# Kernel tuning notes

Hardware: AMD Instinct MI355X
Metric: run time of the kernel (lower is better)

The kernel has to match this reference:

```python
import jax, jax.numpy as jnp
import numpy as np

D_MODEL = 256
D_STATE = 64
NGROUPS = 2
EXPAND = 4
HEADDIM = 128
D_CONV = 4
D_INNER = EXPAND * D_MODEL              # 1024
NHEADS = D_INNER // HEADDIM             # 8
GN = NGROUPS * D_STATE                  # 128
D_IN_PROJ = 2 * D_INNER + 2 * GN + NHEADS  # 2312
EPS = 1e-5


def setup_inputs() -> dict:
    key = jax.random.key(0)
    ks = jax.random.split(key, 12)
    B, L = 2, 4096
    u = jax.random.normal(ks[0], (B, L, D_MODEL), dtype=jnp.float32)
    ln_gamma = jnp.ones((D_MODEL,), jnp.float32)
    ln_beta = jnp.zeros((D_MODEL,), jnp.float32)
    W_in = jax.random.normal(ks[1], (D_MODEL, D_IN_PROJ), jnp.float32) / np.sqrt(D_MODEL)
    conv_w = jax.random.normal(ks[2], (D_INNER + 2 * GN, D_CONV), jnp.float32) * 0.2
    conv_b = jax.random.normal(ks[3], (D_INNER + 2 * GN,), jnp.float32) * 0.02
    dt_bias = jnp.log(jnp.expm1(jax.random.uniform(ks[4], (NHEADS,), jnp.float32, 0.001, 0.1)))
    A_log = jnp.log(jax.random.uniform(ks[5], (NHEADS,), jnp.float32, 1.0, 16.0))
    D_param = jnp.ones((NHEADS,), jnp.float32)
    B_head_scale = jnp.ones((NHEADS, GN), jnp.float32) + 0.02 * jax.random.normal(ks[6], (NHEADS, GN), jnp.float32)
    rms_weight = jnp.ones((D_INNER,), jnp.float32)
    W_out = jax.random.normal(ks[7], (D_INNER, D_MODEL), jnp.float32) / np.sqrt(D_INNER)
    return dict(u=u, ln_gamma=ln_gamma, ln_beta=ln_beta, W_in=W_in, conv_w=conv_w,
                conv_b=conv_b, dt_bias=dt_bias, A_log=A_log, D_param=D_param,
                B_head_scale=B_head_scale, rms_weight=rms_weight, W_out=W_out)


def _mamba_mes(xn, W_in, conv_w, conv_b, dt_bias, A_log, D_param, B_head_scale, rms_weight, W_out):
    B, L, _ = xn.shape
    H, P, K = NHEADS, HEADDIM, D_CONV
    zxbcdt = xn @ W_in                                   # (B,L,2312)
    z = zxbcdt[..., :D_INNER]
    xBC = zxbcdt[..., D_INNER:D_INNER + D_INNER + 2 * GN]
    dt = zxbcdt[..., -H:]
    dt_pos = jax.nn.softplus(dt + dt_bias)               # (B,L,H)
    # causal depthwise conv1d + silu
    xp = jnp.pad(xBC, ((0, 0), (K - 1, 0), (0, 0)))
    conv = sum(xp[:, k:k + L, :] * conv_w[:, k] for k in range(K)) + conv_b
    xBC = jax.nn.silu(conv)
    x = xBC[..., :D_INNER]
    B_shared = xBC[..., D_INNER:D_INNER + GN]            # (B,L,GN)
    C_shared = xBC[..., D_INNER + GN:]                   # (B,L,GN)
    # MES: per-head B via diagonal scale, shared x (mean over heads) and shared C
    B_h = B_shared[:, :, None, :] * B_head_scale[None, None]          # (B,L,H,GN)
    x_shared = x.reshape(B, L, H, P).mean(axis=2)                     # (B,L,P)
    A = -jnp.exp(A_log)                                               # (H,)
    dA = jnp.exp(dt_pos * A)                                          # (B,L,H)
    # selective scan; per-head state (GN, P)
    def step(state, inp):
        dA_t, dt_t, B_t, C_t, x_t = inp   # (B,H),(B,H),(B,H,GN),(B,GN),(B,P)
        state = dA_t[:, :, None, None] * state + jnp.einsum('bh,bhn,bp->bhnp', dt_t, B_t, x_t)
        y_t = jnp.einsum('bn,bhnp->bhp', C_t, state)
        return state, y_t
    init = jnp.zeros((B, H, GN, P), xn.dtype)
    xs = (jnp.moveaxis(dA, 1, 0), jnp.moveaxis(dt_pos, 1, 0), jnp.moveaxis(B_h, 1, 0),
          jnp.moveaxis(C_shared, 1, 0), jnp.moveaxis(x_shared, 1, 0))
    _, ys = jax.lax.scan(step, init, xs)
    y = jnp.moveaxis(ys, 0, 1)                                        # (B,L,H,P)
    y = y + D_param[None, None, :, None] * x_shared[:, :, None, :]    # skip term D*x
    y = y.reshape(B, L, D_INNER)
    # gated RMSNorm: y * silu(z), then rmsnorm
    yg = y * jax.nn.silu(z)
    y = yg * jax.lax.rsqrt(jnp.mean(yg * yg, axis=-1, keepdims=True) + EPS) * rms_weight
    return y @ W_out


def reference(u, ln_gamma, ln_beta, W_in, conv_w, conv_b, dt_bias, A_log,
              D_param, B_head_scale, rms_weight, W_out):
    # pre-LayerNorm
    mu = jnp.mean(u, axis=-1, keepdims=True)
    var = jnp.mean((u - mu) ** 2, axis=-1, keepdims=True)
    xn = (u - mu) * jax.lax.rsqrt(var + EPS) * ln_gamma + ln_beta
    out = _mamba_mes(xn, W_in, conv_w, conv_b, dt_bias, A_log, D_param,
                     B_head_scale, rms_weight, W_out)
    return u + out  # dropout is identity in eval
```

## Files before the change

kernel.cpp:

```cpp
#include <hip/hip_runtime.h>
#include <math.h>

#define LN_TOK 4096
#define NB 2
#define NROWS (NB * LN_TOK)
#define DMODEL 256
#define DINNER 1024
#define NHEADS 8
#define GNN 128
#define DPROJ 2312
#define ZSTRIDE 2432
#define EPSF 1e-5f
#define NCHUNK 32
#define CHUNK 128
#define APAD 72
#define BPAD 64
#define MPAD 136
#define TT 16

typedef unsigned short u16;
typedef unsigned int u32;
typedef __attribute__((ext_vector_type(8))) short shortx8;
typedef __attribute__((ext_vector_type(4))) float floatx4;

__device__ __forceinline__ float sigmoidf_(float v) { return 1.f / (1.f + __expf(-v)); }
__device__ __forceinline__ float siluf_(float v)    { return v / (1.f + __expf(-v)); }
__device__ __forceinline__ float softplusf_(float v){ return v > 20.f ? v : log1pf(__expf(v)); }
__device__ __forceinline__ float b2f(u16 h) { return __uint_as_float(((u32)h) << 16); }
__device__ __forceinline__ u16 f2b(float f) {
    u32 u = __float_as_uint(f);
    u32 r = (u + 0x7fffu + ((u >> 16) & 1u)) >> 16;
    return (u16)r;
}
__device__ __forceinline__ void gld16(const void* g, void* l) {
    __builtin_amdgcn_global_load_lds((const __attribute__((address_space(1))) unsigned int*)g,
                                     (__attribute__((address_space(3))) unsigned int*)l, 16, 0, 0);
}

__global__ void k_ln(const float* __restrict__ u, const float* __restrict__ gam,
                     const float* __restrict__ bet, u16* __restrict__ xn) {
    int row = blockIdx.x;
    int tid = threadIdx.x;
    float v = u[(size_t)row * DMODEL + tid];
    __shared__ float s1[256], s2[256];
    s1[tid] = v; s2[tid] = v * v;
    __syncthreads();
    for (int off = 128; off > 0; off >>= 1) {
        if (tid < off) { s1[tid] += s1[tid + off]; s2[tid] += s2[tid + off]; }
        __syncthreads();
    }
    float mean = s1[0] * (1.f / DMODEL);
    float var  = s2[0] * (1.f / DMODEL) - mean * mean;
    float r = rsqrtf(var + EPSF);
    xn[(size_t)row * DMODEL + tid] = f2b((v - mean) * r * gam[tid] + bet[tid]);
}

__global__ void k_tcast(const float* __restrict__ in, u16* __restrict__ out,
                        int R, int C, int Cp) {
    __shared__ float tile[64][65];
    int c0 = blockIdx.x * 64, r0 = blockIdx.y * 64;
    int tx = threadIdx.x & 63, ty = threadIdx.x >> 6;
    for (int rr = ty; rr < 64; rr += 4) {
        int r = r0 + rr, c = c0 + tx;
        tile[rr][tx] = (r < R && c < C) ? in[(size_t)r * C + c] : 0.f;
    }
    __syncthreads();
    for (int cc = ty; cc < 64; cc += 4) {
        int c = c0 + cc, r = r0 + tx;
        if (c < Cp && r < R) out[(size_t)c * R + r] = f2b(tile[tx][cc]);
    }
}

__global__ __launch_bounds__(256) void k_gemm_bf(const u16* __restrict__ A,
                                                 const u16* __restrict__ Bt,
                                                 u16* __restrict__ C,
                                                 int K, int ldc) {
    __shared__ u16 As[128 * BPAD];
    __shared__ u16 Bs[128 * BPAD];
    int tid = threadIdx.x;
    int wave = tid >> 6, lane = tid & 63;
    int wm = wave >> 1, wn = wave & 1;
    int quad = lane >> 4, l16 = lane & 15;
    int m0 = blockIdx.y * 128, n0 = blockIdx.x * 128;
    floatx4 acc[4][4] = {};
    for (int k0 = 0; k0 < K; k0 += 64) {
#pragma unroll
        for (int p = 0; p < 4; p++) {
            int i = p * 256 + tid;
            int row = i >> 3, kk = (i & 7) << 3;
            gld16(&A[(size_t)(m0 + row) * K + k0 + kk], &As[i * 8]);
            gld16(&Bt[(size_t)(n0 + row) * K + k0 + kk], &Bs[i * 8]);
        }
        __syncthreads();
#pragma unroll
        for (int ks = 0; ks < 64; ks += 32) {
            shortx8 af[4], bfr[4];
#pragma unroll
            for (int i = 0; i < 4; i++)
                af[i] = *(shortx8*)&As[(wm * 64 + i * 16 + l16) * BPAD + ks + (quad << 3)];
#pragma unroll
            for (int j = 0; j < 4; j++)
                bfr[j] = *(shortx8*)&Bs[(wn * 64 + j * 16 + l16) * BPAD + ks + (quad << 3)];
#pragma unroll
            for (int i = 0; i < 4; i++)
#pragma unroll
                for (int j = 0; j < 4; j++)
                    acc[i][j] = __builtin_amdgcn_mfma_f32_16x16x32_bf16(af[i], bfr[j], acc[i][j], 0, 0, 0);
        }
        __syncthreads();
    }
#pragma unroll
    for (int i = 0; i < 4; i++) {
        int row = m0 + wm * 64 + i * 16 + quad * 4;
#pragma unroll
        for (int j = 0; j < 4; j++) {
            int col = n0 + wn * 64 + j * 16 + l16;
#pragma unroll
            for (int r = 0; r < 4; r++)
                C[(size_t)(row + r) * ldc + col] = f2b(acc[i][j][r]);
        }
    }
}

__global__ __launch_bounds__(256) void k_gemm2(const u16* __restrict__ A,
                                               const u16* __restrict__ Bt,
                                               float* __restrict__ C,
                                               int K, int ldc,
                                               const float* __restrict__ addC) {
    __shared__ u16 As[128 * BPAD];
    __shared__ u16 Bs[64 * BPAD];
    int tid = threadIdx.x;
    int wave = tid >> 6, lane = tid & 63;
    int wm = wave >> 1, wn = wave & 1;
    int quad = lane >> 4, l16 = lane & 15;
    int m0 = blockIdx.y * 128, n0 = blockIdx.x * 64;
    floatx4 acc[4][2] = {};
    for (int k0 = 0; k0 < K; k0 += 64) {
#pragma unroll
        for (int p = 0; p < 4; p++) {
            int i = p * 256 + tid;
            int row = i >> 3, kk = (i & 7) << 3;
            gld16(&A[(size_t)(m0 + row) * K + k0 + kk], &As[i * 8]);
        }
#pragma unroll
        for (int p = 0; p < 2; p++) {
            int i = p * 256 + tid;
            int row = i >> 3, kk = (i & 7) << 3;
            gld16(&Bt[(size_t)(n0 + row) * K + k0 + kk], &Bs[i * 8]);
        }
        __syncthreads();
#pragma unroll
        for (int ks = 0; ks < 64; ks += 32) {
            shortx8 af[4], bfr[2];
#pragma unroll
            for (int i = 0; i < 4; i++)
                af[i] = *(shortx8*)&As[(wm * 64 + i * 16 + l16) * BPAD + ks + (quad << 3)];
#pragma unroll
            for (int j = 0; j < 2; j++)
                bfr[j] = *(shortx8*)&Bs[(wn * 32 + j * 16 + l16) * BPAD + ks + (quad << 3)];
#pragma unroll
            for (int i = 0; i < 4; i++)
#pragma unroll
                for (int j = 0; j < 2; j++)
                    acc[i][j] = __builtin_amdgcn_mfma_f32_16x16x32_bf16(af[i], bfr[j], acc[i][j], 0, 0, 0);
        }
        __syncthreads();
    }
#pragma unroll
    for (int i = 0; i < 4; i++) {
        int row = m0 + wm * 64 + i * 16 + quad * 4;
#pragma unroll
        for (int j = 0; j < 2; j++) {
            int col = n0 + wn * 32 + j * 16 + l16;
#pragma unroll
            for (int r = 0; r < 4; r++) {
                size_t idx = (size_t)(row + r) * ldc + col;
                float v = acc[i][j][r];
                if (addC) v += addC[idx];
                C[idx] = v;
            }
        }
    }
}

#define LDW 1296
__global__ __launch_bounds__(256) void k_conv(const u16* __restrict__ zxb,
                                              const float* __restrict__ cw,
                                              const float* __restrict__ cb,
                                              const float* __restrict__ dt_bias,
                                              const float* __restrict__ A_log,
                                              u16* __restrict__ xsh, u16* __restrict__ Bsh,
                                              u16* __restrict__ Csh, u16* __restrict__ XT,
                                              u16* __restrict__ BT,
                                              float* __restrict__ dtp, float* __restrict__ laa) {
    int blk = blockIdx.x;
    int b = blk / (LN_TOK / TT), tile = blk % (LN_TOK / TT);
    int t0 = tile * TT;
    int tid = threadIdx.x;
    __shared__ u16 ld[(TT + 3) * LDW];
    __shared__ float sv[TT][260];
    __shared__ u16 bcv[TT][132];

    for (int i = tid; i < (TT + 3) * 161; i += 256) {
        int r = i / 161, ch = (i % 161) * 8;
        int t = t0 - 3 + r;
        int4 v = make_int4(0, 0, 0, 0);
        if (t >= 0)
            v = *(const int4*)&zxb[((size_t)(b * LN_TOK + t)) * ZSTRIDE + DINNER + ch];
        *(int4*)&ld[r * LDW + ch] = v;
    }

    int cmap[5];
#pragma unroll
    for (int k = 0; k < 4; k++) cmap[k] = (tid >> 7) * 512 + (tid & 127) + 128 * k;
    cmap[4] = 1024 + tid;
    float w0[5], w1[5], w2[5], w3[5], bias[5];
#pragma unroll
    for (int k = 0; k < 5; k++) {
        int c = cmap[k];
        w0[k] = cw[c * 4 + 0]; w1[k] = cw[c * 4 + 1];
        w2[k] = cw[c * 4 + 2]; w3[k] = cw[c * 4 + 3];
        bias[k] = cb[c];
    }
    float dtb = 0.f, negA = 0.f;
    if (tid < NHEADS) { dtb = dt_bias[tid]; negA = -__expf(A_log[tid]); }

    __syncthreads();

    float h1[5], h2[5], h3[5];
#pragma unroll
    for (int k = 0; k < 5; k++) {
        h3[k] = b2f(ld[0 * LDW + cmap[k]]);
        h2[k] = b2f(ld[1 * LDW + cmap[k]]);
        h1[k] = b2f(ld[2 * LDW + cmap[k]]);
    }

    for (int m = 0; m < TT; m++) {
        int t = t0 + m;
        size_t rowp = (size_t)(b * LN_TOK + t) * GNN;
        float xpart = 0.f;
#pragma unroll
        for (int k = 0; k < 5; k++) {
            float cur = b2f(ld[(m + 3) * LDW + cmap[k]]);
            float conv = bias[k] + w3[k] * cur + w2[k] * h1[k] + w1[k] * h2[k] + w0[k] * h3[k];
            h3[k] = h2[k]; h2[k] = h1[k]; h1[k] = cur;
            float s = siluf_(conv);
            if (k < 4) xpart += s;
            else {
                u16 sb = f2b(s);
                if (tid < 128) { Bsh[rowp + tid] = sb; bcv[m][tid] = sb; }
                else           Csh[rowp + tid - 128] = sb;
            }
        }
        sv[m][tid] = xpart;
        if (tid < NHEADS) {
            float dtv = b2f(ld[(m + 3) * LDW + 1280 + tid]) + dtb;
            float dp = softplusf_(dtv);
            size_t idx = ((size_t)(b * NHEADS + tid)) * LN_TOK + t;
            dtp[idx] = dp;
            laa[idx] = negA * dp;
        }
    }
    __syncthreads();

    for (int idx = tid; idx < TT * 128; idx += 256) {
        int m = idx >> 7, p = idx & 127;
        xsh[(size_t)(b * LN_TOK + t0 + m) * GNN + p] =
            f2b((sv[m][p] + sv[m][p + 128]) * 0.125f);
    }
    {
        int p = tid & 127, tg = tid >> 7;
        u16 ox[8], ob[8];
#pragma unroll
        for (int j = 0; j < 8; j++) {
            int m = tg * 8 + j;
            ox[j] = f2b((sv[m][p] + sv[m][p + 128]) * 0.125f);
            ob[j] = bcv[m][p];
        }
        size_t base = ((size_t)(b * GNN + p)) * LN_TOK + t0 + tg * 8;
        int4 vx = make_int4((u32)ox[0] | ((u32)ox[1] << 16), (u32)ox[2] | ((u32)ox[3] << 16),
                            (u32)ox[4] | ((u32)ox[5] << 16), (u32)ox[6] | ((u32)ox[7] << 16));
        int4 vb = make_int4((u32)ob[0] | ((u32)ob[1] << 16), (u32)ob[2] | ((u32)ob[3] << 16),
                            (u32)ob[4] | ((u32)ob[5] << 16), (u32)ob[6] | ((u32)ob[7] << 16));
        *(int4*)&XT[base] = vx;
        *(int4*)&BT[base] = vb;
    }
}

__global__ void k_prefix(const float* __restrict__ laa, float* __restrict__ gcum) {
    int blk = blockIdx.x;
    int bh = blk / NCHUNK, c = blk % NCHUNK;
    int tid = threadIdx.x;
    __shared__ float s[128];
    size_t base = (size_t)bh * LN_TOK + c * CHUNK;
    s[tid] = laa[base + tid];
    __syncthreads();
    for (int off = 1; off < 128; off <<= 1) {
        float v = (tid >= off) ? s[tid - off] : 0.f;
        __syncthreads();
        s[tid] += v;
        __syncthreads();
    }
    gcum[base + tid] = s[tid];
}

__global__ __launch_bounds__(256) void k_chunkS(const u16* __restrict__ BT,
                                                const u16* __restrict__ XT,
                                                const float* __restrict__ scale,
                                                const float* __restrict__ gcum,
                                                const float* __restrict__ dtp,
                                                u16* __restrict__ states) {
    int blk = blockIdx.x;
    int c = blk & 31, h = (blk >> 5) & 7, b = blk >> 8;
    int t0 = c * CHUNK;
    __shared__ u16 As[128 * APAD];
    __shared__ u16 Bs[128 * APAD];
    __shared__ float esc[128], scl[128];
    int tid = threadIdx.x;
    int wave = tid >> 6, lane = tid & 63;
    int wm = wave >> 1, wn = wave & 1;
    int quad = lane >> 4, l16 = lane & 15;
    size_t bhbase = (size_t)(b * NHEADS + h) * LN_TOK + t0;
    if (tid < 128) {
        float gl = gcum[bhbase + 127];
        esc[tid] = __expf(gl - gcum[bhbase + tid]) * dtp[bhbase + tid];
        scl[tid] = scale[h * GNN + tid];
    }
    __syncthreads();
    floatx4 acc[4][4] = {};
    size_t tbase = (size_t)(b * GNN) * LN_TOK + t0;
    for (int k0 = 0; k0 < 128; k0 += 64) {
#pragma unroll
        for (int p = 0; p < 4; p++) {
            int i = p * 256 + tid;
            int row = i >> 3, kk = (i & 7) << 3;
            int4 raw = *(const int4*)&BT[tbase + (size_t)row * LN_TOK + k0 + kk];
            u16* rp = (u16*)&raw;
            float sr = scl[row];
            u32 w[4];
#pragma unroll
            for (int q = 0; q < 4; q++) {
                u16 a  = f2b(b2f(rp[2 * q])     * sr * esc[k0 + kk + 2 * q]);
                u16 bb = f2b(b2f(rp[2 * q + 1]) * sr * esc[k0 + kk + 2 * q + 1]);
                w[q] = (u32)a | ((u32)bb << 16);
            }
            *(int4*)&As[row * APAD + kk] = make_int4(w[0], w[1], w[2], w[3]);
            *(int4*)&Bs[row * APAD + kk] = *(const int4*)&XT[tbase + (size_t)row * LN_TOK + k0 + kk];
        }
        __syncthreads();
#pragma unroll
        for (int ks = 0; ks < 64; ks += 32) {
            shortx8 af[4], bfr[4];
#pragma unroll
            for (int i = 0; i < 4; i++)
                af[i] = *(shortx8*)&As[(wm * 64 + i * 16 + l16) * APAD + ks + (quad << 3)];
#pragma unroll
            for (int j = 0; j < 4; j++)
                bfr[j] = *(shortx8*)&Bs[(wn * 64 + j * 16 + l16) * APAD + ks + (quad << 3)];
#pragma unroll
            for (int i = 0; i < 4; i++)
#pragma unroll
                for (int j = 0; j < 4; j++)
                    acc[i][j] = __builtin_amdgcn_mfma_f32_16x16x32_bf16(af[i], bfr[j], acc[i][j], 0, 0, 0);
        }
        __syncthreads();
    }
    size_t sbase = (size_t)blk * 16384;
#pragma unroll
    for (int i = 0; i < 4; i++) {
        int n0 = wm * 64 + i * 16 + quad * 4;
#pragma unroll
        for (int j = 0; j < 4; j++) {
            int p = wn * 64 + j * 16 + l16;
            u16 o[4];
#pragma unroll
            for (int r = 0; r < 4; r++) o[r] = f2b(acc[i][j][r]);
            u32 lo = (u32)o[0] | ((u32)o[1] << 16);
            u32 hi = (u32)o[2] | ((u32)o[3] << 16);
            *(uint2*)&states[sbase + (size_t)p * CHUNK + n0] = make_uint2(lo, hi);
        }
    }
}

__global__ void k_scan(u16* __restrict__ states, const float* __restrict__ gcum) {
    int idx = blockIdx.x * 256 + threadIdx.x;
    int bh = idx >> 12;
    int np = (idx & 4095) * 4;
    float r0 = 0.f, r1 = 0.f, r2 = 0.f, r3 = 0.f;
    size_t base = (size_t)bh * NCHUNK * 16384 + np;
    size_t gb = (size_t)bh * LN_TOK;
    for (int c = 0; c < NCHUNK; c++) {
        float G = __expf(gcum[gb + c * CHUNK + 127]);
        uint2 v = *(uint2*)&states[base + (size_t)c * 16384];
        float l0 = b2f((u16)(v.x & 0xffff)), l1 = b2f((u16)(v.x >> 16));
        float l2 = b2f((u16)(v.y & 0xffff)), l3 = b2f((u16)(v.y >> 16));
        uint2 o;
        o.x = (u32)f2b(r0) | ((u32)f2b(r1) << 16);
        o.y = (u32)f2b(r2) | ((u32)f2b(r3) << 16);
        *(uint2*)&states[base + (size_t)c * 16384] = o;
        r0 = G * r0 + l0; r1 = G * r1 + l1; r2 = G * r2 + l2; r3 = G * r3 + l3;
    }
}

__global__ __launch_bounds__(256) void k_chunkMY(const u16* __restrict__ Bsh,
                                                 const u16* __restrict__ Csh,
                                                 const float* __restrict__ scale,
                                                 const u16* __restrict__ states,
                                                 const u16* __restrict__ XT,
                                                 const float* __restrict__ gcum,
                                                 const float* __restrict__ dtp,
                                                 u16* __restrict__ y) {
    int blk = blockIdx.x;
    int c = blk & 31, h = (blk >> 5) & 7, b = blk >> 8;
    int t0 = c * CHUNK;
    __shared__ u16 As[128 * APAD];
    __shared__ u16 Bs[128 * APAD];
    __shared__ u16 Mt[128 * MPAD];
    __shared__ float g[128], dts[128], sc[128], eg[128];
    int tid = threadIdx.x;
    int wave = tid >> 6, lane = tid & 63;
    int wm = wave >> 1, wn = wave & 1;
    int quad = lane >> 4, l16 = lane & 15;
    size_t bhbase = (size_t)(b * NHEADS + h) * LN_TOK + t0;
    if (tid < 128) {
        float gv = gcum[bhbase + tid];
        g[tid] = gv;
        eg[tid] = __expf(gv);
        dts[tid] = dtp[bhbase + tid];
        sc[tid] = scale[h * GNN + tid];
    }
    __syncthreads();
    floatx4 acc[4][4] = {};
    size_t rbase = (size_t)(b * LN_TOK + t0) * GNN;
    for (int k0 = 0; k0 < 128; k0 += 64) {
#pragma unroll
        for (int p = 0; p < 4; p++) {
            int i = p * 256 + tid;
            int row = i >> 3, kk = (i & 7) << 3;
            int4 raw = *(const int4*)&Bsh[rbase + (size_t)row * GNN + k0 + kk];
            u16* rp = (u16*)&raw;
            u32 w[4];
#pragma unroll
            for (int q = 0; q < 4; q++) {
                u16 a  = f2b(b2f(rp[2 * q])     * sc[k0 + kk + 2 * q]);
                u16 bb = f2b(b2f(rp[2 * q + 1]) * sc[k0 + kk + 2 * q + 1]);
                w[q] = (u32)a | ((u32)bb << 16);
            }
            *(int4*)&As[row * APAD + kk] = make_int4(w[0], w[1], w[2], w[3]);
            *(int4*)&Bs[row * APAD + kk] = *(const int4*)&Csh[rbase + (size_t)row * GNN + k0 + kk];
        }
        __syncthreads();
#pragma unroll
        for (int ks = 0; ks < 64; ks += 32) {
            shortx8 af[4], bfr[4];
#pragma unroll
            for (int i = 0; i < 4; i++)
                af[i] = *(shortx8*)&As[(wm * 64 + i * 16 + l16) * APAD + ks + (quad << 3)];
#pragma unroll
            for (int j = 0; j < 4; j++)
                bfr[j] = *(shortx8*)&Bs[(wn * 64 + j * 16 + l16) * APAD + ks + (quad << 3)];
#pragma unroll
            for (int i = 0; i < 4; i++)
#pragma unroll
                for (int j = 0; j < 4; j++)
                    acc[i][j] = __builtin_amdgcn_mfma_f32_16x16x32_bf16(af[i], bfr[j], acc[i][j], 0, 0, 0);
        }
        __syncthreads();
    }
#pragma unroll
    for (int i = 0; i < 4; i++) {
        int s0 = wm * 64 + i * 16 + quad * 4;
#pragma unroll
        for (int j = 0; j < 4; j++) {
            int t = wn * 64 + j * 16 + l16;
            u16 o[4];
#pragma unroll
            for (int r = 0; r < 4; r++) {
                int s = s0 + r;
                float v = (s <= t) ? acc[i][j][r] * __expf(g[t] - g[s]) * dts[s] : 0.f;
                o[r] = f2b(v);
            }
            u32 lo = (u32)o[0] | ((u32)o[1] << 16);
            u32 hi = (u32)o[2] | ((u32)o[3] << 16);
            *(uint2*)&Mt[t * MPAD + s0] = make_uint2(lo, hi);
            acc[i][j] = (floatx4){0.f, 0.f, 0.f, 0.f};
        }
    }
    __syncthreads();
    size_t sbase = (size_t)blk * 16384;
    for (int k0 = 0; k0 < 128; k0 += 64) {
#pragma unroll
        for (int p = 0; p < 4; p++) {
            int i = p * 256 + tid;
            int row = i >> 3, kk = (i & 7) << 3;
            int4 raw = *(const int4*)&Csh[rbase + (size_t)row * GNN + k0 + kk];
            float e = eg[row];
            u16* rp = (u16*)&raw;
            u32 w[4];
#pragma unroll
            for (int q = 0; q < 4; q++) {
                u16 a  = f2b(b2f(rp[2 * q]) * e);
                u16 bb = f2b(b2f(rp[2 * q + 1]) * e);
                w[q] = (u32)a | ((u32)bb << 16);
            }
            *(int4*)&As[row * APAD + kk] = make_int4(w[0], w[1], w[2], w[3]);
            *(int4*)&Bs[row * APAD + kk] = *(const int4*)&states[sbase + (size_t)row * CHUNK + k0 + kk];
        }
        __syncthreads();
#pragma unroll
        for (int ks = 0; ks < 64; ks += 32) {
            shortx8 af[4], bfr[4];
#pragma unroll
            for (int i = 0; i < 4; i++)
                af[i] = *(shortx8*)&As[(wm * 64 + i * 16 + l16) * APAD + ks + (quad << 3)];
#pragma unroll
            for (int j = 0; j < 4; j++)
                bfr[j] = *(shortx8*)&Bs[(wn * 64 + j * 16 + l16) * APAD + ks + (quad << 3)];
#pragma unroll
            for (int i = 0; i < 4; i++)
#pragma unroll
                for (int j = 0; j < 4; j++)
                    acc[i][j] = __builtin_amdgcn_mfma_f32_16x16x32_bf16(af[i], bfr[j], acc[i][j], 0, 0, 0);
        }
        __syncthreads();
    }
    size_t xtb = (size_t)(b * GNN) * LN_TOK + t0;
    for (int k0 = 0; k0 < 128; k0 += 64) {
#pragma unroll
        for (int p = 0; p < 4; p++) {
            int i = p * 256 + tid;
            int row = i >> 3, kk = (i & 7) << 3;
            *(int4*)&Bs[row * APAD + kk] = *(const int4*)&XT[xtb + (size_t)row * LN_TOK + k0 + kk];
        }
        __syncthreads();
#pragma unroll
        for (int ks = 0; ks < 64; ks += 32) {
            shortx8 af[4], bfr[4];
#pragma unroll
            for (int i = 0; i < 4; i++)
                af[i] = *(shortx8*)&Mt[(wm * 64 + i * 16 + l16) * MPAD + k0 + ks + (quad << 3)];
#pragma unroll
            for (int j = 0; j < 4; j++)
                bfr[j] = *(shortx8*)&Bs[(wn * 64 + j * 16 + l16) * APAD + ks + (quad << 3)];
#pragma unroll
            for (int i = 0; i < 4; i++)
#pragma unroll
                for (int j = 0; j < 4; j++)
                    acc[i][j] = __builtin_amdgcn_mfma_f32_16x16x32_bf16(af[i], bfr[j], acc[i][j], 0, 0, 0);
        }
        __syncthreads();
    }
#pragma unroll
    for (int i = 0; i < 4; i++) {
        int t = wm * 64 + i * 16 + quad * 4;
#pragma unroll
        for (int j = 0; j < 4; j++) {
            int p = wn * 64 + j * 16 + l16;
#pragma unroll
            for (int r = 0; r < 4; r++)
                y[((size_t)(b * LN_TOK + t0 + t + r)) * DINNER + h * GNN + p] = f2b(acc[i][j][r]);
        }
    }
}

__global__ void k_gate(const u16* __restrict__ y, const u16* __restrict__ zxb,
                       const u16* __restrict__ xsh, const float* __restrict__ Dp,
                       const float* __restrict__ rw, u16* __restrict__ ybuf) {
    int row = blockIdx.x;
    int tid = threadIdx.x;
    size_t yb = (size_t)row * DINNER;
    size_t zb = (size_t)row * ZSTRIDE;
    size_t xb = (size_t)row * GNN;
    float yg[4];
    float ss = 0.f;
#pragma unroll
    for (int q = 0; q < 4; q++) {
        int k = tid * 4 + q;
        int h = k >> 7, p = k & 127;
        float z = b2f(zxb[zb + k]);
        float v = (b2f(y[yb + k]) + Dp[h] * b2f(xsh[xb + p])) * z * sigmoidf_(z);
        yg[q] = v;
        ss += v * v;
    }
    __shared__ float red[256];
    red[tid] = ss;
    __syncthreads();
    for (int off = 128; off > 0; off >>= 1) {
        if (tid < off) red[tid] += red[tid + off];
        __syncthreads();
    }
    float scale = rsqrtf(red[0] * (1.f / DINNER) + EPSF);
#pragma unroll
    for (int q = 0; q < 4; q++) {
        int k = tid * 4 + q;
        ybuf[yb + k] = f2b(yg[q] * scale * rw[k]);
    }
}

extern "C" void kernel_launch(void* const* d_in, const int* in_sizes, int n_in,
                              void* d_out, int out_size, void* d_ws, size_t ws_size,
                              hipStream_t stream) {
    (void)in_sizes; (void)n_in; (void)out_size; (void)ws_size;
    const float* u        = (const float*)d_in[0];
    const float* ln_gamma = (const float*)d_in[1];
    const float* ln_beta  = (const float*)d_in[2];
    const float* W_in     = (const float*)d_in[3];
    const float* conv_w   = (const float*)d_in[4];
    const float* conv_b   = (const float*)d_in[5];
    const float* dt_bias  = (const float*)d_in[6];
    const float* A_log    = (const float*)d_in[7];
    const float* D_param  = (const float*)d_in[8];
    const float* B_scale  = (const float*)d_in[9];
    const float* rms_w    = (const float*)d_in[10];
    const float* W_out    = (const float*)d_in[11];
    float* out = (float*)d_out;

    char* ws = (char*)d_ws;
    u16*   xn_b   = (u16*)ws;                 ws += (size_t)NROWS * DMODEL * 2;
    u16*   Wt     = (u16*)ws;                 ws += (size_t)ZSTRIDE * DMODEL * 2;
    u16*   Wot    = (u16*)ws;                 ws += (size_t)DMODEL * DINNER * 2;
    u16*   zxb    = (u16*)ws;                 ws += (size_t)NROWS * ZSTRIDE * 2;
    u16*   xsh    = (u16*)ws;                 ws += (size_t)NROWS * GNN * 2;
    u16*   Bsh    = (u16*)ws;                 ws += (size_t)NROWS * GNN * 2;
    u16*   Csh    = (u16*)ws;                 ws += (size_t)NROWS * GNN * 2;
    u16*   XT     = (u16*)ws;                 ws += (size_t)NB * GNN * LN_TOK * 2;
    u16*   BT     = (u16*)ws;                 ws += (size_t)NB * GNN * LN_TOK * 2;
    float* dtp    = (float*)ws;               ws += (size_t)NB * NHEADS * LN_TOK * 4;
    float* laa    = (float*)ws;               ws += (size_t)NB * NHEADS * LN_TOK * 4;
    float* gcum   = (float*)ws;               ws += (size_t)NB * NHEADS * LN_TOK * 4;
    u16*   states = (u16*)ws;                 ws += (size_t)512 * 16384 * 2;
    u16*   ybig   = (u16*)ws;                 ws += (size_t)NROWS * DINNER * 2;
    u16*   ybuf   = (u16*)ws;                 ws += (size_t)NROWS * DINNER * 2;

    k_ln<<<NROWS, 256, 0, stream>>>(u, ln_gamma, ln_beta, xn_b);

    k_tcast<<<dim3(ZSTRIDE / 64, DMODEL / 64), 256, 0, stream>>>(W_in, Wt, DMODEL, DPROJ, ZSTRIDE);
    k_tcast<<<dim3(DMODEL / 64, DINNER / 64), 256, 0, stream>>>(W_out, Wot, DINNER, DMODEL, DMODEL);

    k_gemm_bf<<<dim3(ZSTRIDE / 128, NROWS / 128), 256, 0, stream>>>(xn_b, Wt, zxb, DMODEL, ZSTRIDE);

    k_conv<<<NROWS / TT, 256, 0, stream>>>(zxb, conv_w, conv_b, dt_bias, A_log,
                                           xsh, Bsh, Csh, XT, BT, dtp, laa);

    k_prefix<<<NB * NHEADS * NCHUNK, 128, 0, stream>>>(laa, gcum);

    k_chunkS<<<NB * NHEADS * NCHUNK, 256, 0, stream>>>(BT, XT, B_scale, gcum, dtp, states);

    k_scan<<<256, 256, 0, stream>>>(states, gcum);

    k_chunkMY<<<NB * NHEADS * NCHUNK, 256, 0, stream>>>(Bsh, Csh, B_scale, states, XT,
                                                        gcum, dtp, ybig);

    k_gate<<<NROWS, 256, 0, stream>>>(ybig, zxb, xsh, D_param, rms_w, ybuf);

    k_gemm2<<<dim3(DMODEL / 64, NROWS / 128), 256, 0, stream>>>(ybuf, Wot, out, DINNER, DMODEL, u);
}
```

Measured before the change: 226.8 us.

## Fuse prologue kernels, inline chunk prefix sums, widen inter-chunk scan

Merges the LayerNorm and both weight transpose-cast launches into one prologue kernel. The per-chunk cumulative decay is now computed inside chunkS and chunkMY instead of a separate prefix kernel, and chunkS writes only the per-chunk totals. The inter-chunk scan uses twice as many threads, each handling two elements, caches the chunk decays in shared memory and prefetches the next state. This removes three launches and the gcum round trip, at the cost of computing the prefix sum twice.

```diff
diff --git a/kernel.cpp b/kernel.cpp
--- a/kernel.cpp
+++ b/kernel.cpp
@@ -37,37 +37,54 @@
                                      (__attribute__((address_space(3))) unsigned int*)l, 16, 0, 0);
 }
 
-__global__ void k_ln(const float* __restrict__ u, const float* __restrict__ gam,
-                     const float* __restrict__ bet, u16* __restrict__ xn) {
-    int row = blockIdx.x;
+__global__ __launch_bounds__(256) void k_prologue(const float* __restrict__ u,
+                                                  const float* __restrict__ gam,
+                                                  const float* __restrict__ bet,
+                                                  u16* __restrict__ xn,
+                                                  const float* __restrict__ W_in,
+                                                  u16* __restrict__ Wt,
+                                                  const float* __restrict__ W_out,
+                                                  u16* __restrict__ Wot) {
+    __shared__ float smem[64 * 65];
+    int bid = blockIdx.x;
     int tid = threadIdx.x;
-    float v = u[(size_t)row * DMODEL + tid];
-    __shared__ float s1[256], s2[256];
-    s1[tid] = v; s2[tid] = v * v;
-    __syncthreads();
-    for (int off = 128; off > 0; off >>= 1) {
-        if (tid < off) { s1[tid] += s1[tid + off]; s2[tid] += s2[tid + off]; }
-        __syncthreads();
-    }
-    float mean = s1[0] * (1.f / DMODEL);
-    float var  = s2[0] * (1.f / DMODEL) - mean * mean;
-    float r = rsqrtf(var + EPSF);
-    xn[(size_t)row * DMODEL + tid] = f2b((v - mean) * r * gam[tid] + bet[tid]);
-}
-
-__global__ void k_tcast(const float* __restrict__ in, u16* __restrict__ out,
-                        int R, int C, int Cp) {
-    __shared__ float tile[64][65];
-    int c0 = blockIdx.x * 64, r0 = blockIdx.y * 64;
-    int tx = threadIdx.x & 63, ty = threadIdx.x >> 6;
-    for (int rr = ty; rr < 64; rr += 4) {
-        int r = r0 + rr, c = c0 + tx;
-        tile[rr][tx] = (r < R && c < C) ? in[(size_t)r * C + c] : 0.f;
-    }
-    __syncthreads();
-    for (int cc = ty; cc < 64; cc += 4) {
-        int c = c0 + cc, r = r0 + tx;
-        if (c < Cp && r < R) out[(size_t)c * R + r] = f2b(tile[tx][cc]);
+    if (bid < NROWS) {
+        float v = u[(size_t)bid * DMODEL + tid];
+        float* s1 = smem;
+        float* s2 = smem + 256;
+        s1[tid] = v; s2[tid] = v * v;
+        __syncthreads();
+        for (int off = 128; off > 0; off >>= 1) {
+            if (tid < off) { s1[tid] += s1[tid + off]; s2[tid] += s2[tid + off]; }
+            __syncthreads();
+        }
+        float mean = s1[0] * (1.f / DMODEL);
+        float var  = s2[0] * (1.f / DMODEL) - mean * mean;
+        float r = rsqrtf(var + EPSF);
+        xn[(size_t)bid * DMODEL + tid] = f2b((v - mean) * r * gam[tid] + bet[tid]);
+    } else {
+        const float* in; u16* outp; int R, C, Cp, gx, gy;
+        if (bid < NROWS + 152) {
+            int q = bid - NROWS;
+            in = W_in; outp = Wt; R = DMODEL; C = DPROJ; Cp = ZSTRIDE;
+            gx = q % (ZSTRIDE / 64); gy = q / (ZSTRIDE / 64);
+        } else {
+            int q = bid - NROWS - 152;
+            in = W_out; outp = Wot; R = DINNER; C = DMODEL; Cp = DMODEL;
+            gx = q % (DMODEL / 64); gy = q / (DMODEL / 64);
+        }
+        float (*tile)[65] = (float(*)[65])smem;
+        int c0 = gx * 64, r0 = gy * 64;
+        int tx = tid & 63, ty = tid >> 6;
+        for (int rr = ty; rr < 64; rr += 4) {
+            int r = r0 + rr, c = c0 + tx;
+            tile[rr][tx] = (r < R && c < C) ? in[(size_t)r * C + c] : 0.f;
+        }
+        __syncthreads();
+        for (int cc = ty; cc < 64; cc += 4) {
+            int c = c0 + cc, r = r0 + tx;
+            if (c < Cp && r < R) outp[(size_t)c * R + r] = f2b(tile[tx][cc]);
+        }
     }
 }
 
@@ -287,45 +304,39 @@
     }
 }
 
-__global__ void k_prefix(const float* __restrict__ laa, float* __restrict__ gcum) {
-    int blk = blockIdx.x;
-    int bh = blk / NCHUNK, c = blk % NCHUNK;
-    int tid = threadIdx.x;
-    __shared__ float s[128];
-    size_t base = (size_t)bh * LN_TOK + c * CHUNK;
-    s[tid] = laa[base + tid];
-    __syncthreads();
-    for (int off = 1; off < 128; off <<= 1) {
-        float v = (tid >= off) ? s[tid - off] : 0.f;
-        __syncthreads();
-        s[tid] += v;
-        __syncthreads();
-    }
-    gcum[base + tid] = s[tid];
-}
-
 __global__ __launch_bounds__(256) void k_chunkS(const u16* __restrict__ BT,
                                                 const u16* __restrict__ XT,
                                                 const float* __restrict__ scale,
-                                                const float* __restrict__ gcum,
+                                                const float* __restrict__ laa,
                                                 const float* __restrict__ dtp,
-                                                u16* __restrict__ states) {
+                                                u16* __restrict__ states,
+                                                float* __restrict__ gtot) {
     int blk = blockIdx.x;
     int c = blk & 31, h = (blk >> 5) & 7, b = blk >> 8;
     int t0 = c * CHUNK;
     __shared__ u16 As[128 * APAD];
     __shared__ u16 Bs[128 * APAD];
-    __shared__ float esc[128], scl[128];
+    __shared__ float g[128], esc[128], scl[128];
     int tid = threadIdx.x;
     int wave = tid >> 6, lane = tid & 63;
     int wm = wave >> 1, wn = wave & 1;
     int quad = lane >> 4, l16 = lane & 15;
     size_t bhbase = (size_t)(b * NHEADS + h) * LN_TOK + t0;
+    if (tid < 128) g[tid] = laa[bhbase + tid];
+    __syncthreads();
+#pragma unroll
+    for (int off = 1; off < 128; off <<= 1) {
+        float v = 0.f;
+        if (tid < 128 && tid >= off) v = g[tid - off];
+        __syncthreads();
+        if (tid < 128) g[tid] += v;
+        __syncthreads();
+    }
     if (tid < 128) {
-        float gl = gcum[bhbase + 127];
-        esc[tid] = __expf(gl - gcum[bhbase + tid]) * dtp[bhbase + tid];
+        esc[tid] = __expf(g[127] - g[tid]) * dtp[bhbase + tid];
         scl[tid] = scale[h * GNN + tid];
     }
+    if (tid == 0) gtot[(size_t)(b * NHEADS + h) * NCHUNK + c] = g[127];
     __syncthreads();
     floatx4 acc[4][4] = {};
     size_t tbase = (size_t)(b * GNN) * LN_TOK + t0;
@@ -382,23 +393,23 @@
     }
 }
 
-__global__ void k_scan(u16* __restrict__ states, const float* __restrict__ gcum) {
+__global__ void k_scan(u16* __restrict__ states, const float* __restrict__ gtot) {
     int idx = blockIdx.x * 256 + threadIdx.x;
-    int bh = idx >> 12;
-    int np = (idx & 4095) * 4;
-    float r0 = 0.f, r1 = 0.f, r2 = 0.f, r3 = 0.f;
+    int bh = idx >> 13;
+    int np = (idx & 8191) * 2;
+    __shared__ float sG[NCHUNK];
+    if (threadIdx.x < NCHUNK) sG[threadIdx.x] = __expf(gtot[bh * NCHUNK + threadIdx.x]);
+    __syncthreads();
     size_t base = (size_t)bh * NCHUNK * 16384 + np;
-    size_t gb = (size_t)bh * LN_TOK;
+    float r0 = 0.f, r1 = 0.f;
+    u32 v = *(u32*)&states[base];
     for (int c = 0; c < NCHUNK; c++) {
-        float G = __expf(gcum[gb + c * CHUNK + 127]);
-        uint2 v = *(uint2*)&states[base + (size_t)c * 16384];
-        float l0 = b2f((u16)(v.x & 0xffff)), l1 = b2f((u16)(v.x >> 16));
-        float l2 = b2f((u16)(v.y & 0xffff)), l3 = b2f((u16)(v.y >> 16));
-        uint2 o;
-        o.x = (u32)f2b(r0) | ((u32)f2b(r1) << 16);
-        o.y = (u32)f2b(r2) | ((u32)f2b(r3) << 16);
-        *(uint2*)&states[base + (size_t)c * 16384] = o;
-        r0 = G * r0 + l0; r1 = G * r1 + l1; r2 = G * r2 + l2; r3 = G * r3 + l3;
+        u32 vn = (c < NCHUNK - 1) ? *(u32*)&states[base + (size_t)(c + 1) * 16384] : 0u;
+        float l0 = b2f((u16)(v & 0xffff)), l1 = b2f((u16)(v >> 16));
+        *(u32*)&states[base + (size_t)c * 16384] = (u32)f2b(r0) | ((u32)f2b(r1) << 16);
+        float G = sG[c];
+        r0 = G * r0 + l0; r1 = G * r1 + l1;
+        v = vn;
     }
 }
 
@@ -407,7 +418,7 @@
                                                  const float* __restrict__ scale,
                                                  const u16* __restrict__ states,
                                                  const u16* __restrict__ XT,
-                                                 const float* __restrict__ gcum,
+                                                 const float* __restrict__ laa,
                                                  const float* __restrict__ dtp,
                                                  u16* __restrict__ y) {
     int blk = blockIdx.x;
@@ -422,10 +433,18 @@
     int wm = wave >> 1, wn = wave & 1;
     int quad = lane >> 4, l16 = lane & 15;
     size_t bhbase = (size_t)(b * NHEADS + h) * LN_TOK + t0;
+    if (tid < 128) g[tid] = laa[bhbase + tid];
+    __syncthreads();
+#pragma unroll
+    for (int off = 1; off < 128; off <<= 1) {
+        float v = 0.f;
+        if (tid < 128 && tid >= off) v = g[tid - off];
+        __syncthreads();
+        if (tid < 128) g[tid] += v;
+        __syncthreads();
+    }
     if (tid < 128) {
-        float gv = gcum[bhbase + tid];
-        g[tid] = gv;
-        eg[tid] = __expf(gv);
+        eg[tid] = __expf(g[tid]);
         dts[tid] = dtp[bhbase + tid];
         sc[tid] = scale[h * GNN + tid];
     }
@@ -627,29 +646,25 @@
     u16*   BT     = (u16*)ws;                 ws += (size_t)NB * GNN * LN_TOK * 2;
     float* dtp    = (float*)ws;               ws += (size_t)NB * NHEADS * LN_TOK * 4;
     float* laa    = (float*)ws;               ws += (size_t)NB * NHEADS * LN_TOK * 4;
-    float* gcum   = (float*)ws;               ws += (size_t)NB * NHEADS * LN_TOK * 4;
+    float* gtot   = (float*)ws;               ws += (size_t)NB * NHEADS * NCHUNK * 4;
     u16*   states = (u16*)ws;                 ws += (size_t)512 * 16384 * 2;
     u16*   ybig   = (u16*)ws;                 ws += (size_t)NROWS * DINNER * 2;
     u16*   ybuf   = (u16*)ws;                 ws += (size_t)NROWS * DINNER * 2;
 
-    k_ln<<<NROWS, 256, 0, stream>>>(u, ln_gamma, ln_beta, xn_b);
-
-    k_tcast<<<dim3(ZSTRIDE / 64, DMODEL / 64), 256, 0, stream>>>(W_in, Wt, DMODEL, DPROJ, ZSTRIDE);
-    k_tcast<<<dim3(DMODEL / 64, DINNER / 64), 256, 0, stream>>>(W_out, Wot, DINNER, DMODEL, DMODEL);
+    k_prologue<<<NROWS + 152 + 64, 256, 0, stream>>>(u, ln_gamma, ln_beta, xn_b,
+                                                     W_in, Wt, W_out, Wot);
 
     k_gemm_bf<<<dim3(ZSTRIDE / 128, NROWS / 128), 256, 0, stream>>>(xn_b, Wt, zxb, DMODEL, ZSTRIDE);
 
     k_conv<<<NROWS / TT, 256, 0, stream>>>(zxb, conv_w, conv_b, dt_bias, A_log,
                                            xsh, Bsh, Csh, XT, BT, dtp, laa);
 
-    k_prefix<<<NB * NHEADS * NCHUNK, 128, 0, stream>>>(laa, gcum);
-
-    k_chunkS<<<NB * NHEADS * NCHUNK, 256, 0, stream>>>(BT, XT, B_scale, gcum, dtp, states);
-
-    k_scan<<<256, 256, 0, stream>>>(states, gcum);
+    k_chunkS<<<NB * NHEADS * NCHUNK, 256, 0, stream>>>(BT, XT, B_scale, laa, dtp, states, gtot);
+
+    k_scan<<<512, 256, 0, stream>>>(states, gtot);
 
     k_chunkMY<<<NB * NHEADS * NCHUNK, 256, 0, stream>>>(Bsh, Csh, B_scale, states, XT,
-                                                        gcum, dtp, ybig);
+                                                        laa, dtp, ybig);
 
     k_gate<<<NROWS, 256, 0, stream>>>(ybig, zxb, xsh, D_param, rms_w, ybuf);
 
```

Measured after the change: 212.0 us. -6.5%, faster.
